# Performance work log

Measured on AMD Instinct MI355X. Metric: run time of the kernel, lower is better.

The kernel has to match this reference:

```python
import jax, jax.numpy as jnp
import numpy as np

N, IN_F, OUT_F = 8192, 256, 128
ALPHA = 0.2          # LeakyReLU negative slope
NEG_INF = -9e15      # mask value used by the original module
DENSITY = 0.1        # adjacency density


def setup_inputs() -> dict:
    key = jax.random.key(0)
    k1, k2, k3, k4 = jax.random.split(key, 4)
    x = jax.random.normal(k1, (N, IN_F), dtype=jnp.float32)
    adj = (jax.random.uniform(k2, (N, N)) < DENSITY).astype(jnp.float32)
    W = jax.random.normal(k3, (IN_F, OUT_F), dtype=jnp.float32) * (1.0 / np.sqrt(IN_F))
    a = jax.random.normal(k4, (2 * OUT_F, 1), dtype=jnp.float32) * (1.0 / np.sqrt(2 * OUT_F))
    return {"x": x, "adj": adj, "W": W, "a": a}


def reference(x, adj, W, a):
    # h = x @ W : [N, F]
    h = x @ W
    # Decompose a^T [h_i ; h_j] = (h a1)_i + (h a2)_j  -- identical math to the
    # original O(N^2 * 2F) cat/repeat construction, without materializing it.
    a1 = a[:OUT_F, 0]           # [F]
    a2 = a[OUT_F:, 0]           # [F]
    s1 = h @ a1                 # [N]
    s2 = h @ a2                 # [N]
    e = jax.nn.leaky_relu(s1[:, None] + s2[None, :], negative_slope=ALPHA)  # [N, N]
    scores = jnp.where(adj > 0, e, NEG_INF)
    attention = jax.nn.softmax(scores, axis=1)   # row-wise softmax
    # dropout = 0.0 (eval mode) -> identity
    h_prime = attention @ h      # [N, F]
    return h_prime
```

## Files before the change

kernel.cpp:

```cpp
#include <hip/hip_runtime.h>
#include <hip/hip_bf16.h>

typedef __attribute__((ext_vector_type(4))) float  f32x4;
typedef __attribute__((ext_vector_type(8))) short  bf16x8;
typedef unsigned short u16;

#define ALPHA 0.2f
#define NN 8192
#define FF 128
#define LOG2E 1.4426950408889634f

__device__ __forceinline__ u16 f2b(float f) {
  __hip_bfloat16 hb = __float2bfloat16(f);
  return *reinterpret_cast<u16*>(&hb);
}

extern "C" __global__ void __launch_bounds__(256)
wt_cvt(const float* __restrict__ x, const float* __restrict__ Wm,
       u16* __restrict__ xb, u16* __restrict__ WTb) {
  const int id = blockIdx.x * 256 + threadIdx.x;
  if (blockIdx.x < 2048) {
    const f32x4 v = *(const f32x4*)(x + (size_t)id * 4);
    uint2 p;
    p.x = f2b(v.x) | ((unsigned)f2b(v.y) << 16);
    p.y = f2b(v.z) | ((unsigned)f2b(v.w) << 16);
    *(uint2*)(xb + (size_t)id * 4) = p;
  } else {
    const int o = id - 2048 * 256;
    const int c = o >> 8, k = o & 255;
    WTb[o] = f2b(Wm[k * 128 + c]);
  }
}

extern "C" __global__ void __launch_bounds__(256)
gat_h(const u16* __restrict__ xb, const u16* __restrict__ WTb,
      const float* __restrict__ av, u16* __restrict__ hT2,
      float* __restrict__ s1v, float* __restrict__ s2v) {
  __shared__ float hs[16][128];
  const int t = threadIdx.x, lane = t & 63, wv = t >> 6;
  const int i0 = blockIdx.x * 16;
  const int fr = lane & 15, kg = lane >> 4;

  f32x4 acc0 = {0.f,0.f,0.f,0.f}, acc1 = {0.f,0.f,0.f,0.f};
  const u16* xp  = xb  + (size_t)(i0 + fr) * 256 + kg * 8;
  const u16* b0p = WTb + (size_t)(wv * 32 + fr) * 256 + kg * 8;
  const u16* b1p = b0p + 16 * 256;
#pragma unroll
  for (int ks = 0; ks < 8; ++ks) {
    const bf16x8 A  = *(const bf16x8*)(xp  + ks * 32);
    const bf16x8 B0 = *(const bf16x8*)(b0p + ks * 32);
    const bf16x8 B1 = *(const bf16x8*)(b1p + ks * 32);
    acc0 = __builtin_amdgcn_mfma_f32_16x16x32_bf16(A, B0, acc0, 0, 0, 0);
    acc1 = __builtin_amdgcn_mfma_f32_16x16x32_bf16(A, B1, acc1, 0, 0, 0);
  }
#pragma unroll
  for (int r = 0; r < 4; ++r) {
    hs[kg * 4 + r][wv * 32 + fr]      = acc0[r];
    hs[kg * 4 + r][wv * 32 + 16 + fr] = acc1[r];
  }
  __syncthreads();

  {
    const int c = t >> 1, rr = (t & 1) * 8;
    u16 u[8];
#pragma unroll
    for (int m = 0; m < 8; ++m) u[m] = f2b(hs[rr + m][c]);
    *(uint4*)(hT2 + ((size_t)(i0 >> 5) * 128 + c) * 32 + (i0 & 31) + rr) =
        *(const uint4*)u;
  }
  {
    const int r = t >> 4, q = t & 15;
    float p1 = 0.f, p2 = 0.f;
#pragma unroll
    for (int m = 0; m < 8; ++m) {
      const int c = q * 8 + m;
      const float hv = hs[r][c];
      p1 = fmaf(hv, av[c], p1);
      p2 = fmaf(hv, av[128 + c], p2);
    }
    p1 += __shfl_xor(p1, 1); p1 += __shfl_xor(p1, 2);
    p1 += __shfl_xor(p1, 4); p1 += __shfl_xor(p1, 8);
    p2 += __shfl_xor(p2, 1); p2 += __shfl_xor(p2, 2);
    p2 += __shfl_xor(p2, 4); p2 += __shfl_xor(p2, 8);
    if (q == 0) { s1v[i0 + r] = p1 * LOG2E; s2v[i0 + r] = p2 * LOG2E; }
  }
}

#define MM(BB, AA) AA = __builtin_amdgcn_mfma_f32_16x16x32_bf16(af0, BB, AA, 0, 0, 0)
#define MM1(BB, AA) AA = __builtin_amdgcn_mfma_f32_16x16x32_bf16(af1, BB, AA, 0, 0, 0)

extern "C" __global__ void __launch_bounds__(256, 4)
gat_main(const float* __restrict__ adj, const u16* __restrict__ hT2,
         const float* __restrict__ s1l, const float* __restrict__ s2l,
         float* __restrict__ nump, float* __restrict__ deng) {
  __shared__ float accp[4][16][132];
  __shared__ float denp[4][16];

  const int t = threadIdx.x, lane = t & 63, ks = t >> 6;
  const int fr = lane & 15, kg = lane >> 4;
  const int tile = blockIdx.x >> 2, q = blockIdx.x & 3;
  const int i0 = tile * 32;
  const int jq = q * 2048;

  const float s1i0 = s1l[i0 + fr];
  const float s1i1 = s1l[i0 + 16 + fr];
  const float* adjp0 = adj + (size_t)(i0 + fr) * NN + jq + ks * 32 + kg * 8;
  const float* adjp1 = adjp0 + (size_t)16 * NN;
  const float* s2p   = s2l + jq + ks * 32 + kg * 8;
  const u16*   hp    = hT2 + (size_t)(q * 64 + ks) * 4096 + fr * 32 + kg * 8;

  f32x4 acc0[8], acc1[8];
#pragma unroll
  for (int f = 0; f < 8; ++f) { acc0[f] = (f32x4){0,0,0,0}; acc1[f] = (f32x4){0,0,0,0}; }
  float den0 = 0.f, den1 = 0.f;

  f32x4 a0 = *(const f32x4*)(adjp0);
  f32x4 a1 = *(const f32x4*)(adjp0 + 4);
  f32x4 a2 = *(const f32x4*)(adjp1);
  f32x4 a3 = *(const f32x4*)(adjp1 + 4);
  f32x4 z0 = *(const f32x4*)(s2p);
  f32x4 z1 = *(const f32x4*)(s2p + 4);

  for (int it = 0; it < 16; ++it) {
    const u16* hb = hp + it * 16384;
    const bf16x8 b0 = *(const bf16x8*)(hb);
    const bf16x8 b1 = *(const bf16x8*)(hb + 512);
    const bf16x8 b2 = *(const bf16x8*)(hb + 1024);
    const bf16x8 b3 = *(const bf16x8*)(hb + 1536);
    __builtin_amdgcn_sched_barrier(0);

    bf16x8 af0, af1;
    float d0 = 0.f, d1 = 0.f;
#pragma unroll
    for (int e = 0; e < 8; ++e) {
      const float zz  = (e < 4) ? z0[e] : z1[e - 4];
      const float av0 = (e < 4) ? a0[e] : a1[e - 4];
      const float av1 = (e < 4) ? a2[e] : a3[e - 4];
      float t0 = s1i0 + zz; t0 = fmaxf(t0, ALPHA * t0);
      float t1 = s1i1 + zz; t1 = fmaxf(t1, ALPHA * t1);
      const float w0 = av0 * exp2f(t0);
      const float w1 = av1 * exp2f(t1);
      d0 += w0; d1 += w1;
      af0[e] = (short)f2b(w0);
      af1[e] = (short)f2b(w1);
    }
    den0 += d0; den1 += d1;
    __builtin_amdgcn_sched_barrier(0);

    const bf16x8 b4 = *(const bf16x8*)(hb + 2048);
    const bf16x8 b5 = *(const bf16x8*)(hb + 2560);
    const bf16x8 b6 = *(const bf16x8*)(hb + 3072);
    const bf16x8 b7 = *(const bf16x8*)(hb + 3584);
    __builtin_amdgcn_sched_barrier(0);

    MM(b0, acc0[0]); MM1(b0, acc1[0]); MM(b1, acc0[1]); MM1(b1, acc1[1]);
    MM(b2, acc0[2]); MM1(b2, acc1[2]); MM(b3, acc0[3]); MM1(b3, acc1[3]);

    const int itn = it < 15 ? it + 1 : 15;
    a0 = *(const f32x4*)(adjp0 + itn * 128);
    a1 = *(const f32x4*)(adjp0 + itn * 128 + 4);
    a2 = *(const f32x4*)(adjp1 + itn * 128);
    a3 = *(const f32x4*)(adjp1 + itn * 128 + 4);
    z0 = *(const f32x4*)(s2p + itn * 128);
    z1 = *(const f32x4*)(s2p + itn * 128 + 4);
    __builtin_amdgcn_sched_barrier(0);

    MM(b4, acc0[4]); MM1(b4, acc1[4]); MM(b5, acc0[5]); MM1(b5, acc1[5]);
    MM(b6, acc0[6]); MM1(b6, acc1[6]); MM(b7, acc0[7]); MM1(b7, acc1[7]);
  }

  const size_t obase = ((size_t)(q * 256 + tile)) * 32;

  {
    float d = den0;
    d += __shfl_xor(d, 16); d += __shfl_xor(d, 32);
    if (lane < 16) denp[ks][fr] = d;
#pragma unroll
    for (int f = 0; f < 8; ++f)
#pragma unroll
      for (int r = 0; r < 4; ++r) accp[ks][kg * 4 + r][f * 16 + fr] = acc0[f][r];
    __syncthreads();
    const int row = t >> 4, c0 = (t & 15) * 8;
    f32x4 sA = {0,0,0,0}, sB = {0,0,0,0};
#pragma unroll
    for (int w = 0; w < 4; ++w) {
      sA += *(const f32x4*)&accp[w][row][c0];
      sB += *(const f32x4*)&accp[w][row][c0 + 4];
    }
    float* op = nump + (obase + row) * FF + c0;
    *(f32x4*)op = sA; *(f32x4*)(op + 4) = sB;
    if ((t & 15) == 0)
      deng[obase + row] = denp[0][row] + denp[1][row] + denp[2][row] + denp[3][row];
    __syncthreads();
  }
  {
    float d = den1;
    d += __shfl_xor(d, 16); d += __shfl_xor(d, 32);
    if (lane < 16) denp[ks][fr] = d;
#pragma unroll
    for (int f = 0; f < 8; ++f)
#pragma unroll
      for (int r = 0; r < 4; ++r) accp[ks][kg * 4 + r][f * 16 + fr] = acc1[f][r];
    __syncthreads();
    const int row = t >> 4, c0 = (t & 15) * 8;
    f32x4 sA = {0,0,0,0}, sB = {0,0,0,0};
#pragma unroll
    for (int w = 0; w < 4; ++w) {
      sA += *(const f32x4*)&accp[w][row][c0];
      sB += *(const f32x4*)&accp[w][row][c0 + 4];
    }
    float* op = nump + (obase + 16 + row) * FF + c0;
    *(f32x4*)op = sA; *(f32x4*)(op + 4) = sB;
    if ((t & 15) == 0)
      deng[obase + 16 + row] = denp[0][row] + denp[1][row] + denp[2][row] + denp[3][row];
  }
}

extern "C" __global__ void __launch_bounds__(256)
gat_red(const float* __restrict__ nump, const float* __restrict__ deng,
        float* __restrict__ out) {
  const int gid = blockIdx.x * 256 + threadIdx.x;
  const int i = gid >> 5, c4 = (gid & 31) * 4;
  const int tile = i >> 5, row = i & 31;
  f32x4 s = {0,0,0,0};
  float dv = 0.f;
#pragma unroll
  for (int q = 0; q < 4; ++q) {
    const size_t rb = ((size_t)(q * 256 + tile)) * 32 + row;
    s  += *(const f32x4*)(nump + rb * FF + c4);
    dv += deng[rb];
  }
  const float inv = 1.f / dv;
  s *= inv;
  *(f32x4*)(out + (size_t)i * FF + c4) = s;
}

extern "C" void kernel_launch(void* const* d_in, const int* in_sizes, int n_in,
                              void* d_out, int out_size, void* d_ws, size_t ws_size,
                              hipStream_t stream) {
  const float* x   = (const float*)d_in[0];
  const float* adj = (const float*)d_in[1];
  const float* Wm  = (const float*)d_in[2];
  const float* av  = (const float*)d_in[3];
  float* out = (float*)d_out;

  char* ws = (char*)d_ws;
  u16*   hT2 = (u16*)(ws);
  float* s1v = (float*)(ws + 2097152);
  float* s2v = (float*)(ws + 2129920);
  u16*   xb  = (u16*)(ws + 2162688);
  u16*   WTb = (u16*)(ws + 6356992);
  float* nump = (float*)(ws + 6422528);
  float* deng = (float*)(ws + 23199744);

  wt_cvt  <<<2176, 256, 0, stream>>>(x, Wm, xb, WTb);
  gat_h   <<<NN / 16, 256, 0, stream>>>(xb, WTb, av, hT2, s1v, s2v);
  gat_main<<<1024, 256, 0, stream>>>(adj, hT2, s1v, s2v, nump, deng);
  gat_red <<<1024, 256, 0, stream>>>(nump, deng, out);
}
```

Measured before the change: 454.8 us.

## Prefetch adjacency two iterations ahead with double-buffered registers in gat_main

Deepens the software pipeline for the adjacency stream. Adjacency loads are now issued two iterations ahead into alternating even and odd register sets, and the loop is unrolled by two to use them. All eight h fragment loads are also hoisted to the start of each step. The added live registers force the occupancy hint down from 4 to 3 blocks per CU, trading latency hiding through occupancy for latency hiding through prefetch.

```diff
diff --git a/kernel.cpp b/kernel.cpp
--- a/kernel.cpp
+++ b/kernel.cpp
@@ -89,7 +89,7 @@
 #define MM(BB, AA) AA = __builtin_amdgcn_mfma_f32_16x16x32_bf16(af0, BB, AA, 0, 0, 0)
 #define MM1(BB, AA) AA = __builtin_amdgcn_mfma_f32_16x16x32_bf16(af1, BB, AA, 0, 0, 0)
 
-extern "C" __global__ void __launch_bounds__(256, 4)
+extern "C" __global__ void __launch_bounds__(256, 3)
 gat_main(const float* __restrict__ adj, const u16* __restrict__ hT2,
          const float* __restrict__ s1l, const float* __restrict__ s2l,
          float* __restrict__ nump, float* __restrict__ deng) {
@@ -114,19 +114,27 @@
   for (int f = 0; f < 8; ++f) { acc0[f] = (f32x4){0,0,0,0}; acc1[f] = (f32x4){0,0,0,0}; }
   float den0 = 0.f, den1 = 0.f;
 
-  f32x4 a0 = *(const f32x4*)(adjp0);
-  f32x4 a1 = *(const f32x4*)(adjp0 + 4);
-  f32x4 a2 = *(const f32x4*)(adjp1);
-  f32x4 a3 = *(const f32x4*)(adjp1 + 4);
-  f32x4 z0 = *(const f32x4*)(s2p);
-  f32x4 z1 = *(const f32x4*)(s2p + 4);
-
-  for (int it = 0; it < 16; ++it) {
+  f32x4 aE0 = *(const f32x4*)(adjp0);
+  f32x4 aE1 = *(const f32x4*)(adjp0 + 4);
+  f32x4 aE2 = *(const f32x4*)(adjp1);
+  f32x4 aE3 = *(const f32x4*)(adjp1 + 4);
+  f32x4 aO0 = *(const f32x4*)(adjp0 + 128);
+  f32x4 aO1 = *(const f32x4*)(adjp0 + 132);
+  f32x4 aO2 = *(const f32x4*)(adjp1 + 128);
+  f32x4 aO3 = *(const f32x4*)(adjp1 + 132);
+  f32x4 z0  = *(const f32x4*)(s2p);
+  f32x4 z1  = *(const f32x4*)(s2p + 4);
+
+  auto step = [&](f32x4& A0, f32x4& A1, f32x4& A2, f32x4& A3, int it) {
     const u16* hb = hp + it * 16384;
     const bf16x8 b0 = *(const bf16x8*)(hb);
     const bf16x8 b1 = *(const bf16x8*)(hb + 512);
     const bf16x8 b2 = *(const bf16x8*)(hb + 1024);
     const bf16x8 b3 = *(const bf16x8*)(hb + 1536);
+    const bf16x8 b4 = *(const bf16x8*)(hb + 2048);
+    const bf16x8 b5 = *(const bf16x8*)(hb + 2560);
+    const bf16x8 b6 = *(const bf16x8*)(hb + 3072);
+    const bf16x8 b7 = *(const bf16x8*)(hb + 3584);
     __builtin_amdgcn_sched_barrier(0);
 
     bf16x8 af0, af1;
@@ -134,8 +142,8 @@
 #pragma unroll
     for (int e = 0; e < 8; ++e) {
       const float zz  = (e < 4) ? z0[e] : z1[e - 4];
-      const float av0 = (e < 4) ? a0[e] : a1[e - 4];
-      const float av1 = (e < 4) ? a2[e] : a3[e - 4];
+      const float av0 = (e < 4) ? A0[e] : A1[e - 4];
+      const float av1 = (e < 4) ? A2[e] : A3[e - 4];
       float t0 = s1i0 + zz; t0 = fmaxf(t0, ALPHA * t0);
       float t1 = s1i1 + zz; t1 = fmaxf(t1, ALPHA * t1);
       const float w0 = av0 * exp2f(t0);
@@ -147,26 +155,25 @@
     den0 += d0; den1 += d1;
     __builtin_amdgcn_sched_barrier(0);
 
-    const bf16x8 b4 = *(const bf16x8*)(hb + 2048);
-    const bf16x8 b5 = *(const bf16x8*)(hb + 2560);
-    const bf16x8 b6 = *(const bf16x8*)(hb + 3072);
-    const bf16x8 b7 = *(const bf16x8*)(hb + 3584);
+    const int ia = it + 2 < 16 ? it + 2 : 15;
+    const int iz = it + 1 < 16 ? it + 1 : 15;
+    A0 = *(const f32x4*)(adjp0 + ia * 128);
+    A1 = *(const f32x4*)(adjp0 + ia * 128 + 4);
+    A2 = *(const f32x4*)(adjp1 + ia * 128);
+    A3 = *(const f32x4*)(adjp1 + ia * 128 + 4);
+    z0 = *(const f32x4*)(s2p + iz * 128);
+    z1 = *(const f32x4*)(s2p + iz * 128 + 4);
     __builtin_amdgcn_sched_barrier(0);
 
     MM(b0, acc0[0]); MM1(b0, acc1[0]); MM(b1, acc0[1]); MM1(b1, acc1[1]);
     MM(b2, acc0[2]); MM1(b2, acc1[2]); MM(b3, acc0[3]); MM1(b3, acc1[3]);
-
-    const int itn = it < 15 ? it + 1 : 15;
-    a0 = *(const f32x4*)(adjp0 + itn * 128);
-    a1 = *(const f32x4*)(adjp0 + itn * 128 + 4);
-    a2 = *(const f32x4*)(adjp1 + itn * 128);
-    a3 = *(const f32x4*)(adjp1 + itn * 128 + 4);
-    z0 = *(const f32x4*)(s2p + itn * 128);
-    z1 = *(const f32x4*)(s2p + itn * 128 + 4);
-    __builtin_amdgcn_sched_barrier(0);
-
     MM(b4, acc0[4]); MM1(b4, acc1[4]); MM(b5, acc0[5]); MM1(b5, acc1[5]);
     MM(b6, acc0[6]); MM1(b6, acc1[6]); MM(b7, acc0[7]); MM1(b7, acc1[7]);
+  };
+
+  for (int m = 0; m < 8; ++m) {
+    step(aE0, aE1, aE2, aE3, 2 * m);
+    step(aO0, aO1, aO2, aO3, 2 * m + 1);
   }
 
   const size_t obase = ((size_t)(q * 256 + tile)) * 32;
```

New measurement: 636.2 us. +39.9%, slower.

## Stage adjacency tiles into LDS via async global_load_lds double buffering

Applied to the files above, without the earlier changes.

Adjacency rows are no longer loaded straight into registers with one-iteration register prefetch. They are now copied asynchronously from global memory into a double-buffered LDS pool using global_load_lds, with coalesced full-row 16-byte loads per wave. Each wave then reads its fragment from LDS, and the loop is restructured as a stage/compute pipeline with a barrier per iteration. The shared pool is reused for the reduction scratch, and launch bounds drop the occupancy hint from 4 to 3 blocks per CU. This trades an extra LDS round trip and block-wide barriers for better-coalesced, asynchronous adjacency streaming.

```diff
diff --git a/kernel.cpp b/kernel.cpp
--- a/kernel.cpp
+++ b/kernel.cpp
@@ -9,6 +9,8 @@
 #define NN 8192
 #define FF 128
 #define LOG2E 1.4426950408889634f
+#define AS1 __attribute__((address_space(1)))
+#define AS3 __attribute__((address_space(3)))
 
 __device__ __forceinline__ u16 f2b(float f) {
   __hip_bfloat16 hb = __float2bfloat16(f);
@@ -89,12 +91,11 @@
 #define MM(BB, AA) AA = __builtin_amdgcn_mfma_f32_16x16x32_bf16(af0, BB, AA, 0, 0, 0)
 #define MM1(BB, AA) AA = __builtin_amdgcn_mfma_f32_16x16x32_bf16(af1, BB, AA, 0, 0, 0)
 
-extern "C" __global__ void __launch_bounds__(256, 4)
+extern "C" __global__ void __launch_bounds__(256, 3)
 gat_main(const float* __restrict__ adj, const u16* __restrict__ hT2,
          const float* __restrict__ s1l, const float* __restrict__ s2l,
          float* __restrict__ nump, float* __restrict__ deng) {
-  __shared__ float accp[4][16][132];
-  __shared__ float denp[4][16];
+  __shared__ __align__(16) char pool[34048];
 
   const int t = threadIdx.x, lane = t & 63, ks = t >> 6;
   const int fr = lane & 15, kg = lane >> 4;
@@ -104,29 +105,48 @@
 
   const float s1i0 = s1l[i0 + fr];
   const float s1i1 = s1l[i0 + 16 + fr];
-  const float* adjp0 = adj + (size_t)(i0 + fr) * NN + jq + ks * 32 + kg * 8;
-  const float* adjp1 = adjp0 + (size_t)16 * NN;
-  const float* s2p   = s2l + jq + ks * 32 + kg * 8;
-  const u16*   hp    = hT2 + (size_t)(q * 64 + ks) * 4096 + fr * 32 + kg * 8;
+  const float* s2p = s2l + jq + ks * 32 + kg * 8;
+  const u16*   hp  = hT2 + (size_t)(q * 64 + ks) * 4096 + fr * 32 + kg * 8;
+
+  const int drow = ks * 8 + (lane >> 5);
+  const float* gp0 = adj + (size_t)(i0 + drow + 0) * NN + jq + (lane & 31) * 4;
+  const float* gp2 = gp0 + (size_t)2 * NN;
+  const float* gp4 = gp0 + (size_t)4 * NN;
+  const float* gp6 = gp0 + (size_t)6 * NN;
 
   f32x4 acc0[8], acc1[8];
 #pragma unroll
   for (int f = 0; f < 8; ++f) { acc0[f] = (f32x4){0,0,0,0}; acc1[f] = (f32x4){0,0,0,0}; }
   float den0 = 0.f, den1 = 0.f;
 
-  f32x4 a0 = *(const f32x4*)(adjp0);
-  f32x4 a1 = *(const f32x4*)(adjp0 + 4);
-  f32x4 a2 = *(const f32x4*)(adjp1);
-  f32x4 a3 = *(const f32x4*)(adjp1 + 4);
-  f32x4 z0 = *(const f32x4*)(s2p);
-  f32x4 z1 = *(const f32x4*)(s2p + 4);
-
-  for (int it = 0; it < 16; ++it) {
-    const u16* hb = hp + it * 16384;
+  auto STAGE = [&](int buf, int tt) {
+    char* lb = pool + buf * 16384 + ks * 4096;
+    const size_t off = (size_t)tt * 128;
+    __builtin_amdgcn_global_load_lds((const AS1 void*)(gp0 + off), (AS3 void*)(lb       ), 16, 0, 0);
+    __builtin_amdgcn_global_load_lds((const AS1 void*)(gp2 + off), (AS3 void*)(lb + 1024), 16, 0, 0);
+    __builtin_amdgcn_global_load_lds((const AS1 void*)(gp4 + off), (AS3 void*)(lb + 2048), 16, 0, 0);
+    __builtin_amdgcn_global_load_lds((const AS1 void*)(gp6 + off), (AS3 void*)(lb + 3072), 16, 0, 0);
+    __builtin_amdgcn_sched_barrier(0);
+  };
+
+  auto COMPUTE = [&](int buf, int tt) {
+    const f32x4 z0 = *(const f32x4*)(s2p + tt * 128);
+    const f32x4 z1 = *(const f32x4*)(s2p + tt * 128 + 4);
+    const u16* hb = hp + (size_t)tt * 16384;
     const bf16x8 b0 = *(const bf16x8*)(hb);
     const bf16x8 b1 = *(const bf16x8*)(hb + 512);
     const bf16x8 b2 = *(const bf16x8*)(hb + 1024);
     const bf16x8 b3 = *(const bf16x8*)(hb + 1536);
+    const bf16x8 b4 = *(const bf16x8*)(hb + 2048);
+    const bf16x8 b5 = *(const bf16x8*)(hb + 2560);
+    const bf16x8 b6 = *(const bf16x8*)(hb + 3072);
+    const bf16x8 b7 = *(const bf16x8*)(hb + 3584);
+    const char* ab = pool + buf * 16384;
+    const int cb = ks * 128 + kg * 32;
+    const f32x4 x0 = *(const f32x4*)(ab + fr * 512 + cb);
+    const f32x4 x1 = *(const f32x4*)(ab + fr * 512 + cb + 16);
+    const f32x4 x2 = *(const f32x4*)(ab + (16 + fr) * 512 + cb);
+    const f32x4 x3 = *(const f32x4*)(ab + (16 + fr) * 512 + cb + 16);
     __builtin_amdgcn_sched_barrier(0);
 
     bf16x8 af0, af1;
@@ -134,8 +154,8 @@
 #pragma unroll
     for (int e = 0; e < 8; ++e) {
       const float zz  = (e < 4) ? z0[e] : z1[e - 4];
-      const float av0 = (e < 4) ? a0[e] : a1[e - 4];
-      const float av1 = (e < 4) ? a2[e] : a3[e - 4];
+      const float av0 = (e < 4) ? x0[e] : x1[e - 4];
+      const float av1 = (e < 4) ? x2[e] : x3[e - 4];
       float t0 = s1i0 + zz; t0 = fmaxf(t0, ALPHA * t0);
       float t1 = s1i1 + zz; t1 = fmaxf(t1, ALPHA * t1);
       const float w0 = av0 * exp2f(t0);
@@ -145,36 +165,32 @@
       af1[e] = (short)f2b(w1);
     }
     den0 += d0; den1 += d1;
-    __builtin_amdgcn_sched_barrier(0);
-
-    const bf16x8 b4 = *(const bf16x8*)(hb + 2048);
-    const bf16x8 b5 = *(const bf16x8*)(hb + 2560);
-    const bf16x8 b6 = *(const bf16x8*)(hb + 3072);
-    const bf16x8 b7 = *(const bf16x8*)(hb + 3584);
-    __builtin_amdgcn_sched_barrier(0);
 
     MM(b0, acc0[0]); MM1(b0, acc1[0]); MM(b1, acc0[1]); MM1(b1, acc1[1]);
     MM(b2, acc0[2]); MM1(b2, acc1[2]); MM(b3, acc0[3]); MM1(b3, acc1[3]);
-
-    const int itn = it < 15 ? it + 1 : 15;
-    a0 = *(const f32x4*)(adjp0 + itn * 128);
-    a1 = *(const f32x4*)(adjp0 + itn * 128 + 4);
-    a2 = *(const f32x4*)(adjp1 + itn * 128);
-    a3 = *(const f32x4*)(adjp1 + itn * 128 + 4);
-    z0 = *(const f32x4*)(s2p + itn * 128);
-    z1 = *(const f32x4*)(s2p + itn * 128 + 4);
-    __builtin_amdgcn_sched_barrier(0);
-
     MM(b4, acc0[4]); MM1(b4, acc1[4]); MM(b5, acc0[5]); MM1(b5, acc1[5]);
     MM(b6, acc0[6]); MM1(b6, acc1[6]); MM(b7, acc0[7]); MM1(b7, acc1[7]);
-  }
+  };
+
+  STAGE(0, 0);
+  __syncthreads();
+  for (int tt = 0; tt < 15; ++tt) {
+    STAGE((tt + 1) & 1, tt + 1);
+    COMPUTE(tt & 1, tt);
+    __syncthreads();
+  }
+  COMPUTE(1, 15);
+  __syncthreads();
+
+  float (*accp)[16][132] = (float (*)[16][132])(void*)pool;
+  float* denp = (float*)(pool + 33792);
 
   const size_t obase = ((size_t)(q * 256 + tile)) * 32;
 
   {
     float d = den0;
     d += __shfl_xor(d, 16); d += __shfl_xor(d, 32);
-    if (lane < 16) denp[ks][fr] = d;
+    if (lane < 16) denp[ks * 16 + fr] = d;
 #pragma unroll
     for (int f = 0; f < 8; ++f)
 #pragma unroll
@@ -190,13 +206,13 @@
     float* op = nump + (obase + row) * FF + c0;
     *(f32x4*)op = sA; *(f32x4*)(op + 4) = sB;
     if ((t & 15) == 0)
-      deng[obase + row] = denp[0][row] + denp[1][row] + denp[2][row] + denp[3][row];
+      deng[obase + row] = denp[row] + denp[16 + row] + denp[32 + row] + denp[48 + row];
     __syncthreads();
   }
   {
     float d = den1;
     d += __shfl_xor(d, 16); d += __shfl_xor(d, 32);
-    if (lane < 16) denp[ks][fr] = d;
+    if (lane < 16) denp[ks * 16 + fr] = d;
 #pragma unroll
     for (int f = 0; f < 8; ++f)
 #pragma unroll
@@ -212,7 +228,7 @@
     float* op = nump + (obase + 16 + row) * FF + c0;
     *(f32x4*)op = sA; *(f32x4*)(op + 4) = sB;
     if ((t & 15) == 0)
-      deng[obase + 16 + row] = denp[0][row] + denp[1][row] + denp[2][row] + denp[3][row];
+      deng[obase + 16 + row] = denp[row] + denp[16 + row] + denp[32 + row] + denp[48 + row];
   }
 }
 
```

Result: faster. 388.1 us (-14.7%).

## Pack adjacency into bitmask pre-pass and feed bit masks to main kernel

Applied to the files above, without the earlier changes.

A new adj_pack kernel streams the dense float adjacency once and uses wave ballots to write a 1-bit-per-entry mask. gat_main then reads compact 32-bit mask words instead of 8 floats per lane per step, selecting exp2 or zero by bit test in place of multiplying by the adjacency value. The main loop is restructured into a double-buffered even/odd step, prefetching the next mask words and s2 values, and occupancy is lowered from 4 to 3 blocks per CU. The full adjacency read still happens every call but now runs as a separate pass that cannot overlap with the compute in gat_main, which adds an extra launch.

```diff
diff --git a/kernel.cpp b/kernel.cpp
--- a/kernel.cpp
+++ b/kernel.cpp
@@ -4,6 +4,8 @@
 typedef __attribute__((ext_vector_type(4))) float  f32x4;
 typedef __attribute__((ext_vector_type(8))) short  bf16x8;
 typedef unsigned short u16;
+typedef unsigned int u32;
+typedef unsigned long long u64;
 
 #define ALPHA 0.2f
 #define NN 8192
@@ -33,6 +35,28 @@
 }
 
 extern "C" __global__ void __launch_bounds__(256)
+adj_pack(const float* __restrict__ adj, u64* __restrict__ mask) {
+  const int lane = threadIdx.x & 63;
+  const size_t base = ((size_t)blockIdx.x * 4 + (threadIdx.x >> 6)) * 256;
+  for (int s = 0; s < 256; s += 4) {
+    const float v0 = adj[(base + s + 0) * 64 + lane];
+    const float v1 = adj[(base + s + 1) * 64 + lane];
+    const float v2 = adj[(base + s + 2) * 64 + lane];
+    const float v3 = adj[(base + s + 3) * 64 + lane];
+    const u64 b0 = __ballot(v0 > 0.0f);
+    const u64 b1 = __ballot(v1 > 0.0f);
+    const u64 b2 = __ballot(v2 > 0.0f);
+    const u64 b3 = __ballot(v3 > 0.0f);
+    if (lane == 0) {
+      mask[base + s + 0] = b0;
+      mask[base + s + 1] = b1;
+      mask[base + s + 2] = b2;
+      mask[base + s + 3] = b3;
+    }
+  }
+}
+
+extern "C" __global__ void __launch_bounds__(256)
 gat_h(const u16* __restrict__ xb, const u16* __restrict__ WTb,
       const float* __restrict__ av, u16* __restrict__ hT2,
       float* __restrict__ s1v, float* __restrict__ s2v) {
@@ -89,8 +113,8 @@
 #define MM(BB, AA) AA = __builtin_amdgcn_mfma_f32_16x16x32_bf16(af0, BB, AA, 0, 0, 0)
 #define MM1(BB, AA) AA = __builtin_amdgcn_mfma_f32_16x16x32_bf16(af1, BB, AA, 0, 0, 0)
 
-extern "C" __global__ void __launch_bounds__(256, 4)
-gat_main(const float* __restrict__ adj, const u16* __restrict__ hT2,
+extern "C" __global__ void __launch_bounds__(256, 3)
+gat_main(const u32* __restrict__ pmask, const u16* __restrict__ hT2,
          const float* __restrict__ s1l, const float* __restrict__ s2l,
          float* __restrict__ nump, float* __restrict__ deng) {
   __shared__ float accp[4][16][132];
@@ -104,69 +128,68 @@
 
   const float s1i0 = s1l[i0 + fr];
   const float s1i1 = s1l[i0 + 16 + fr];
-  const float* adjp0 = adj + (size_t)(i0 + fr) * NN + jq + ks * 32 + kg * 8;
-  const float* adjp1 = adjp0 + (size_t)16 * NN;
-  const float* s2p   = s2l + jq + ks * 32 + kg * 8;
-  const u16*   hp    = hT2 + (size_t)(q * 64 + ks) * 4096 + fr * 32 + kg * 8;
+  const float* s2p = s2l + jq + ks * 32 + kg * 8;
+  const u16*   hp  = hT2 + (size_t)(q * 64 + ks) * 4096 + fr * 32 + kg * 8;
+  const u32* pm0 = pmask + (size_t)(i0 + fr) * 256 + q * 64 + ks;
+  const u32* pm1 = pm0 + 16 * 256;
+  const int msh = kg * 8;
 
   f32x4 acc0[8], acc1[8];
 #pragma unroll
   for (int f = 0; f < 8; ++f) { acc0[f] = (f32x4){0,0,0,0}; acc1[f] = (f32x4){0,0,0,0}; }
   float den0 = 0.f, den1 = 0.f;
 
-  f32x4 a0 = *(const f32x4*)(adjp0);
-  f32x4 a1 = *(const f32x4*)(adjp0 + 4);
-  f32x4 a2 = *(const f32x4*)(adjp1);
-  f32x4 a3 = *(const f32x4*)(adjp1 + 4);
-  f32x4 z0 = *(const f32x4*)(s2p);
-  f32x4 z1 = *(const f32x4*)(s2p + 4);
-
-  for (int it = 0; it < 16; ++it) {
-    const u16* hb = hp + it * 16384;
+  u32  mE0 = pm0[0], mE1 = pm1[0];
+  f32x4 zE0 = *(const f32x4*)(s2p);
+  f32x4 zE1 = *(const f32x4*)(s2p + 4);
+  u32 mO0, mO1; f32x4 zO0, zO1;
+
+  auto stepf = [&](u32& mc0, u32& mc1, f32x4& zc0, f32x4& zc1,
+                   u32& mn0, u32& mn1, f32x4& zn0, f32x4& zn1, int tt) {
+    const u16* hb = hp + (size_t)tt * 16384;
     const bf16x8 b0 = *(const bf16x8*)(hb);
     const bf16x8 b1 = *(const bf16x8*)(hb + 512);
     const bf16x8 b2 = *(const bf16x8*)(hb + 1024);
     const bf16x8 b3 = *(const bf16x8*)(hb + 1536);
-    __builtin_amdgcn_sched_barrier(0);
-
-    bf16x8 af0, af1;
-    float d0 = 0.f, d1 = 0.f;
-#pragma unroll
-    for (int e = 0; e < 8; ++e) {
-      const float zz  = (e < 4) ? z0[e] : z1[e - 4];
-      const float av0 = (e < 4) ? a0[e] : a1[e - 4];
-      const float av1 = (e < 4) ? a2[e] : a3[e - 4];
-      float t0 = s1i0 + zz; t0 = fmaxf(t0, ALPHA * t0);
-      float t1 = s1i1 + zz; t1 = fmaxf(t1, ALPHA * t1);
-      const float w0 = av0 * exp2f(t0);
-      const float w1 = av1 * exp2f(t1);
-      d0 += w0; d1 += w1;
-      af0[e] = (short)f2b(w0);
-      af1[e] = (short)f2b(w1);
-    }
-    den0 += d0; den1 += d1;
-    __builtin_amdgcn_sched_barrier(0);
-
     const bf16x8 b4 = *(const bf16x8*)(hb + 2048);
     const bf16x8 b5 = *(const bf16x8*)(hb + 2560);
     const bf16x8 b6 = *(const bf16x8*)(hb + 3072);
     const bf16x8 b7 = *(const bf16x8*)(hb + 3584);
     __builtin_amdgcn_sched_barrier(0);
 
+    const int tn = tt + 1 < 16 ? tt + 1 : 15;
+    mn0 = pm0[tn * 4];
+    mn1 = pm1[tn * 4];
+    zn0 = *(const f32x4*)(s2p + tn * 128);
+    zn1 = *(const f32x4*)(s2p + tn * 128 + 4);
+    __builtin_amdgcn_sched_barrier(0);
+
+    const u32 ms0 = mc0 >> msh;
+    const u32 ms1 = mc1 >> msh;
+    bf16x8 af0, af1;
+    float d0 = 0.f, d1 = 0.f;
+#pragma unroll
+    for (int e = 0; e < 8; ++e) {
+      const float zz = (e < 4) ? zc0[e] : zc1[e - 4];
+      float t0 = s1i0 + zz; t0 = fmaxf(t0, ALPHA * t0);
+      float t1 = s1i1 + zz; t1 = fmaxf(t1, ALPHA * t1);
+      const float w0 = (ms0 & (1u << e)) ? exp2f(t0) : 0.0f;
+      const float w1 = (ms1 & (1u << e)) ? exp2f(t1) : 0.0f;
+      d0 += w0; d1 += w1;
+      af0[e] = (short)f2b(w0);
+      af1[e] = (short)f2b(w1);
+    }
+    den0 += d0; den1 += d1;
+
     MM(b0, acc0[0]); MM1(b0, acc1[0]); MM(b1, acc0[1]); MM1(b1, acc1[1]);
     MM(b2, acc0[2]); MM1(b2, acc1[2]); MM(b3, acc0[3]); MM1(b3, acc1[3]);
-
-    const int itn = it < 15 ? it + 1 : 15;
-    a0 = *(const f32x4*)(adjp0 + itn * 128);
-    a1 = *(const f32x4*)(adjp0 + itn * 128 + 4);
-    a2 = *(const f32x4*)(adjp1 + itn * 128);
-    a3 = *(const f32x4*)(adjp1 + itn * 128 + 4);
-    z0 = *(const f32x4*)(s2p + itn * 128);
-    z1 = *(const f32x4*)(s2p + itn * 128 + 4);
-    __builtin_amdgcn_sched_barrier(0);
-
     MM(b4, acc0[4]); MM1(b4, acc1[4]); MM(b5, acc0[5]); MM1(b5, acc1[5]);
     MM(b6, acc0[6]); MM1(b6, acc1[6]); MM(b7, acc0[7]); MM1(b7, acc1[7]);
+  };
+
+  for (int m = 0; m < 8; ++m) {
+    stepf(mE0, mE1, zE0, zE1, mO0, mO1, zO0, zO1, 2 * m);
+    stepf(mO0, mO1, zO0, zO1, mE0, mE1, zE0, zE1, 2 * m + 1);
   }
 
   const size_t obase = ((size_t)(q * 256 + tile)) * 32;
@@ -252,9 +275,11 @@
   u16*   WTb = (u16*)(ws + 6356992);
   float* nump = (float*)(ws + 6422528);
   float* deng = (float*)(ws + 23199744);
-
+  u64*   mask = (u64*)(ws + 23330816);
+
+  adj_pack<<<1024, 256, 0, stream>>>(adj, mask);
   wt_cvt  <<<2176, 256, 0, stream>>>(x, Wm, xb, WTb);
   gat_h   <<<NN / 16, 256, 0, stream>>>(xb, WTb, av, hT2, s1v, s2v);
-  gat_main<<<1024, 256, 0, stream>>>(adj, hT2, s1v, s2v, nump, deng);
+  gat_main<<<1024, 256, 0, stream>>>((const u32*)mask, hT2, s1v, s2v, nump, deng);
   gat_red <<<1024, 256, 0, stream>>>(nump, deng, out);
 }
```

Result: slower. 502.4 us (+10.5%).
